# Performance work log

Hardware: AMD Instinct MI355X
Metric: run time of the kernel (lower is better)

The kernel has to match this reference:

```python
import jax, jax.numpy as jnp
import numpy as np

T, D, H, E, K = 8192, 1024, 1024, 8, 2
N = T * K  # total dispatched rows


def setup_inputs() -> dict:
    key = jax.random.key(0)
    ks = jax.random.split(key, 12)
    s = 1.0 / np.sqrt(D)
    inp = {
        # uniform, contiguous per-expert segments: 2048 rows each
        'offsets': jnp.arange(E + 1, dtype=jnp.int64 if jax.config.jax_enable_x64 else jnp.int32) * (N // E),
        'jagged': jax.random.normal(ks[0], (T, D), jnp.float32),
        'weight': jax.random.normal(ks[1], (E, D, H), jnp.float32) * s,
        'bias': jax.random.normal(ks[2], (E, H), jnp.float32) * 0.02,
        'index': jax.random.randint(ks[3], (N,), 0, T),
        'weight_p': jax.random.normal(ks[4], (E, D, H), jnp.float32) * s,
        'weight_out': jax.random.normal(ks[5], (E, H, D), jnp.float32) * (1.0 / np.sqrt(H)),
        'reverse_index': jax.random.randint(ks[6], (T, K), 0, N),
        'gates': jax.random.uniform(ks[7], (N,), jnp.float32),
        'gates_index': jax.random.randint(ks[8], (T, K), 0, N),
        'bias_p': jax.random.normal(ks[9], (E, H), jnp.float32) * 0.02,
        'bias_out': jax.random.normal(ks[10], (E, D), jnp.float32) * 0.02,
    }
    return inp


def reference(offsets, jagged, weight, bias, index, weight_p, weight_out,
              reverse_index, gates, gates_index, bias_p, bias_out):
    # dispatch: gather token features into expert-sorted order  [N, D]
    x = jagged[index]
    n = x.shape[0]
    n_experts = weight.shape[0]
    # contiguous segment id per dispatched row
    expert_id = jnp.searchsorted(offsets, jnp.arange(n), side='right') - 1
    y = jnp.zeros((n, weight_out.shape[-1]), dtype=x.dtype)
    for e in range(n_experts):  # fixed small expert count
        m = (expert_id == e)[:, None].astype(x.dtype)
        xe = x * m
        g = xe @ weight[e] + bias[e]        # gate proj  [N, H]
        u = xe @ weight_p[e] + bias_p[e]    # up proj    [N, H]
        h = jax.nn.silu(g) * u              # SwiGLU
        y = y + (h @ weight_out[e] + bias_out[e]) * m
    # combine: gather K expert outputs per token, weight by gates  [T, D]
    gathered = y[reverse_index]             # [T, K, D]
    gv = gates[gates_index]                 # [T, K]
    return jnp.einsum('tkd,tk->td', gathered, gv)
```

## Files before the change

kernel.cpp:

```cpp
#include <hip/hip_runtime.h>
#include <hip/hip_bf16.h>

#define T_TOK 8192
#define DDIM 1024
#define HDIM 1024
#define NEXP 8
#define KTOP 2
#define NROWS (T_TOK * KTOP)

typedef __attribute__((ext_vector_type(8))) short bf16x8;
typedef __attribute__((ext_vector_type(4))) float f32x4;

__device__ __forceinline__ unsigned short f2bf(float f) {
    unsigned u = __builtin_bit_cast(unsigned, f);
    u += 0x7fffu + ((u >> 16) & 1u);
    return (unsigned short)(u >> 16);
}
__device__ __forceinline__ float bf2f(unsigned short h) {
    return __builtin_bit_cast(float, (unsigned)h << 16);
}

__device__ __forceinline__ void gll16(const unsigned short* g, const unsigned short* l) {
    __builtin_amdgcn_global_load_lds(
        (const __attribute__((address_space(1))) unsigned int*)g,
        (__attribute__((address_space(3))) unsigned int*)l, 16, 0, 0);
}


__global__ __launch_bounds__(256) void cvt_bf16_k(const float* __restrict__ in,
                                                  unsigned short* __restrict__ out, int n4) {
    int i = blockIdx.x * 256 + threadIdx.x;
    if (i >= n4) return;
    float4 v = ((const float4*)in)[i];
    ushort4 o;
    o.x = f2bf(v.x); o.y = f2bf(v.y); o.z = f2bf(v.z); o.w = f2bf(v.w);
    ((ushort4*)out)[i] = o;
}

__global__ __launch_bounds__(256) void transpose_cast_k(const float* __restrict__ in,
                                                        unsigned short* __restrict__ out,
                                                        int R, int C) {
    __shared__ unsigned short tile[32][33];
    int m = blockIdx.z;
    const float* src = in + (size_t)m * R * C;
    unsigned short* dst = out + (size_t)m * R * C;
    int c0 = blockIdx.x * 32, r0 = blockIdx.y * 32;
    int tx = threadIdx.x & 31, ty = threadIdx.x >> 5;
#pragma unroll
    for (int i = 0; i < 32; i += 8)
        tile[ty + i][tx] = f2bf(src[(size_t)(r0 + ty + i) * C + c0 + tx]);
    __syncthreads();
#pragma unroll
    for (int i = 0; i < 32; i += 8)
        dst[(size_t)(c0 + ty + i) * R + r0 + tx] = tile[tx][ty + i];
}


constexpr int BM2 = 256, BN2 = 256, BK2 = 32;
constexpr int NT2 = DDIM / BK2;

template <int VARIANT>
__global__ __launch_bounds__(512) void gemm256_8p_k(
    const unsigned short* __restrict__ A, const int* __restrict__ rowidx, int lda,
    const unsigned short* __restrict__ Bt, const float* __restrict__ biasE,
    const unsigned short* __restrict__ Gin, unsigned short* __restrict__ Out,
    const int* __restrict__ offsets, int N, int K) {
    __shared__ __attribute__((aligned(16))) unsigned short lds[65536];

    const int nbn = N / BN2;
    int l = (blockIdx.x & 7) * 32 + (blockIdx.x >> 3);
    int brow = l / nbn, bcol = l % nbn;
    int row0 = brow * BM2, col0 = bcol * BN2;
    int e = 0;
    while (offsets[e + 1] <= row0) ++e;

    const unsigned short* Bte = Bt + (size_t)e * N * K;
    const float* bias = biasE + (size_t)e * N;

    int tid = threadIdx.x;
    int lane = tid & 63, wid = tid >> 6;
    int wm = wid >> 2, wn = wid & 3;
    int l15 = lane & 15, l4 = lane >> 4;

    int sc = (lane & 7) ^ (lane >> 3);
    int srow = ((lane >> 3) << 1) + (sc >> 2);
    int scol = (sc & 3) * 8;
    const unsigned short* asrc[2];
    const unsigned short* bsrc[2];
#pragma unroll
    for (int q = 0; q < 2; ++q) {
        int gr = row0 + (wid * 2 + q) * 16 + srow;
        int ar = rowidx ? rowidx[gr] : gr;
        asrc[q] = A + (size_t)ar * lda + scol;
        bsrc[q] = Bte + (size_t)(col0 + (wid * 2 + q) * 16 + srow) * K + scol;
    }
    unsigned adst[2], bdst[2];
#pragma unroll
    for (int q = 0; q < 2; ++q) {
        adst[q] = (wid * 2 + q) * 512;
        bdst[q] = 32768 + (wid * 2 + q) * 512;
    }

#define STAGE_A(t) { int _b = (t) & 3; int _k = (t) * BK2;            \
        gll16(asrc[0] + _k, lds + _b * 8192 + adst[0]);               \
        gll16(asrc[1] + _k, lds + _b * 8192 + adst[1]); }
#define STAGE_B(t) { int _b = (t) & 3; int _k = (t) * BK2;            \
        gll16(bsrc[0] + _k, lds + _b * 8192 + bdst[0]);               \
        gll16(bsrc[1] + _k, lds + _b * 8192 + bdst[1]); }

    int rdoff = (l15 >> 1) * 128 + ((((l15 & 1) << 2) | l4) ^ (l15 >> 1)) * 16;

    f32x4 acc[8][4] = {};

    STAGE_A(0) STAGE_B(0) STAGE_A(1) STAGE_B(1) STAGE_A(2) STAGE_B(2)
    asm volatile("s_waitcnt vmcnt(8)" ::: "memory");
    __builtin_amdgcn_s_barrier();

#pragma unroll 1
    for (int t = 0; t < NT2; ++t) {
        const char* Ab = (const char*)lds + (t & 3) * 16384;
        const char* Bb = (const char*)lds + 65536 + (t & 3) * 16384;
        bf16x8 af0[4], af1[4], bfr[4];

#pragma unroll
        for (int mi = 0; mi < 4; ++mi)
            af0[mi] = *(const bf16x8*)(Ab + (wm * 64 + mi * 8) * 128 + rdoff);
#pragma unroll
        for (int ni = 0; ni < 4; ++ni)
            bfr[ni] = *(const bf16x8*)(Bb + (wn * 32 + ni * 8) * 128 + rdoff);
        if (t + 3 < NT2) STAGE_A(t + 3)
        __builtin_amdgcn_s_barrier();
        asm volatile("s_waitcnt lgkmcnt(0)" ::: "memory");
        __builtin_amdgcn_sched_barrier(0);
        __builtin_amdgcn_s_setprio(1);
#pragma unroll
        for (int mi = 0; mi < 4; ++mi)
#pragma unroll
            for (int ni = 0; ni < 4; ++ni)
                acc[mi][ni] = __builtin_amdgcn_mfma_f32_16x16x32_bf16(
                    af0[mi], bfr[ni], acc[mi][ni], 0, 0, 0);
        __builtin_amdgcn_s_setprio(0);
        __builtin_amdgcn_s_barrier();

#pragma unroll
        for (int mi = 0; mi < 4; ++mi)
            af1[mi] = *(const bf16x8*)(Ab + (wm * 64 + 32 + mi * 8) * 128 + rdoff);
        if (t + 3 < NT2) STAGE_B(t + 3)
        __builtin_amdgcn_s_barrier();
        asm volatile("s_waitcnt lgkmcnt(0)" ::: "memory");
        __builtin_amdgcn_sched_barrier(0);
        __builtin_amdgcn_s_setprio(1);
#pragma unroll
        for (int mi = 0; mi < 4; ++mi)
#pragma unroll
            for (int ni = 0; ni < 4; ++ni)
                acc[4 + mi][ni] = __builtin_amdgcn_mfma_f32_16x16x32_bf16(
                    af1[mi], bfr[ni], acc[4 + mi][ni], 0, 0, 0);
        __builtin_amdgcn_s_setprio(0);

        if (t < NT2 - 1) {
            if (t <= NT2 - 4)      asm volatile("s_waitcnt vmcnt(8)" ::: "memory");
            else if (t == NT2 - 3) asm volatile("s_waitcnt vmcnt(4)" ::: "memory");
            else                   asm volatile("s_waitcnt vmcnt(0)" ::: "memory");
            __builtin_amdgcn_s_barrier();
        }
    }
#undef STAGE_A
#undef STAGE_B

    float bv[4];
#pragma unroll
    for (int ni = 0; ni < 4; ++ni)
        bv[ni] = bias[col0 + wn * 64 + ni * 16 + l15];

#pragma unroll
    for (int a = 0; a < 8; ++a) {
        int orow_b = row0 + wm * 128 + (a >> 2) * 64 + (a & 3) * 16 + l4 * 4;
#pragma unroll
        for (int ni = 0; ni < 4; ++ni) {
            int ocol = col0 + wn * 64 + ni * 16 + l15;
#pragma unroll
            for (int q = 0; q < 4; ++q) {
                size_t oidx = (size_t)(orow_b + q) * N + ocol;
                float v = acc[a][ni][q] + bv[ni];
                if (VARIANT == 1) {
                    float g = bf2f(Gin[oidx]);
                    float s = g / (1.0f + __expf(-g));
                    v = s * v;
                }
                Out[oidx] = f2bf(v);
            }
        }
    }
}


__global__ __launch_bounds__(256) void combine_k(
    const unsigned short* __restrict__ Y, const int* __restrict__ rev,
    const float* __restrict__ gates, const int* __restrict__ gidx,
    float* __restrict__ out) {
    int t = blockIdx.x;
    int r0 = rev[2 * t], r1 = rev[2 * t + 1];
    float g0 = gates[gidx[2 * t]], g1 = gates[gidx[2 * t + 1]];
    const unsigned short* y0 = Y + (size_t)r0 * DDIM;
    const unsigned short* y1 = Y + (size_t)r1 * DDIM;
    int d = threadIdx.x * 4;
    ushort4 a = *(const ushort4*)(y0 + d);
    ushort4 b = *(const ushort4*)(y1 + d);
    float4 r;
    r.x = g0 * bf2f(a.x) + g1 * bf2f(b.x);
    r.y = g0 * bf2f(a.y) + g1 * bf2f(b.y);
    r.z = g0 * bf2f(a.z) + g1 * bf2f(b.z);
    r.w = g0 * bf2f(a.w) + g1 * bf2f(b.w);
    *(float4*)(out + (size_t)t * DDIM + d) = r;
}


extern "C" void kernel_launch(void* const* d_in, const int* in_sizes, int n_in,
                              void* d_out, int out_size, void* d_ws, size_t ws_size,
                              hipStream_t stream) {
    const int* offsets = (const int*)d_in[0];
    const float* jagged = (const float*)d_in[1];
    const float* weight = (const float*)d_in[2];
    const float* bias = (const float*)d_in[3];
    const int* index = (const int*)d_in[4];
    const float* weight_p = (const float*)d_in[5];
    const float* weight_out = (const float*)d_in[6];
    const int* rev = (const int*)d_in[7];
    const float* gates = (const float*)d_in[8];
    const int* gidx = (const int*)d_in[9];
    const float* bias_p = (const float*)d_in[10];
    const float* bias_out = (const float*)d_in[11];
    float* out = (float*)d_out;

    char* w = (char*)d_ws;
    unsigned short* jag_bf = (unsigned short*)w; w += (size_t)T_TOK * DDIM * 2;
    unsigned short* W1t    = (unsigned short*)w; w += (size_t)NEXP * DDIM * HDIM * 2;
    unsigned short* Wpt    = (unsigned short*)w; w += (size_t)NEXP * DDIM * HDIM * 2;
    unsigned short* Wot    = (unsigned short*)w; w += (size_t)NEXP * HDIM * DDIM * 2;
    unsigned short* g_ws   = (unsigned short*)w; w += (size_t)NROWS * HDIM * 2;
    unsigned short* h_ws   = (unsigned short*)w; w += (size_t)NROWS * HDIM * 2;
    unsigned short* y_ws   = g_ws;

    cvt_bf16_k<<<(T_TOK * DDIM / 4 + 255) / 256, 256, 0, stream>>>(jagged, jag_bf, T_TOK * DDIM / 4);
    transpose_cast_k<<<dim3(HDIM / 32, DDIM / 32, NEXP), 256, 0, stream>>>(weight, W1t, DDIM, HDIM);
    transpose_cast_k<<<dim3(HDIM / 32, DDIM / 32, NEXP), 256, 0, stream>>>(weight_p, Wpt, DDIM, HDIM);
    transpose_cast_k<<<dim3(DDIM / 32, HDIM / 32, NEXP), 256, 0, stream>>>(weight_out, Wot, HDIM, DDIM);

    const int grid = (NROWS / BM2) * (HDIM / BN2);

    gemm256_8p_k<0><<<grid, 512, 0, stream>>>(jag_bf, index, DDIM, W1t, bias, nullptr, g_ws,
                                              offsets, HDIM, DDIM);
    gemm256_8p_k<1><<<grid, 512, 0, stream>>>(jag_bf, index, DDIM, Wpt, bias_p, g_ws, h_ws,
                                              offsets, HDIM, DDIM);
    gemm256_8p_k<0><<<grid, 512, 0, stream>>>(h_ws, nullptr, HDIM, Wot, bias_out, nullptr, y_ws,
                                              offsets, DDIM, HDIM);
    combine_k<<<T_TOK, 256, 0, stream>>>(y_ws, rev, gates, gidx, out);
}
```

Before: 183.0 us.

## Collapse two-phase ping-pong K-loop into single-barrier loop per k-tile

Replaces the 8-phase style inner loop, which split each k-tile into two half-MFMA phases with staggered A/B staging and several barriers, with a simpler loop. The new loop issues all staging loads up front, reads all 8 A fragments and 4 B fragments, runs all 32 MFMAs, and then uses one wait-and-barrier per tile. The aim is to cut barrier count and scheduling overhead. In exchange it gives up the interleaving of LDS reads, global loads and MFMAs between waves, uses more fragment registers, and may leave MFMA units idle during the LDS reads.

```diff
diff --git a/kernel.cpp b/kernel.cpp
--- a/kernel.cpp
+++ b/kernel.cpp
@@ -60,7 +60,7 @@
 constexpr int NT2 = DDIM / BK2;
 
 template <int VARIANT>
-__global__ __launch_bounds__(512) void gemm256_8p_k(
+__global__ __launch_bounds__(512) void gemm256_1b_k(
     const unsigned short* __restrict__ A, const int* __restrict__ rowidx, int lda,
     const unsigned short* __restrict__ Bt, const float* __restrict__ biasE,
     const unsigned short* __restrict__ Gin, unsigned short* __restrict__ Out,
@@ -101,10 +101,9 @@
         bdst[q] = 32768 + (wid * 2 + q) * 512;
     }
 
-#define STAGE_A(t) { int _b = (t) & 3; int _k = (t) * BK2;            \
+#define STAGE(t) { int _b = (t) & 3; int _k = (t) * BK2;              \
         gll16(asrc[0] + _k, lds + _b * 8192 + adst[0]);               \
-        gll16(asrc[1] + _k, lds + _b * 8192 + adst[1]); }
-#define STAGE_B(t) { int _b = (t) & 3; int _k = (t) * BK2;            \
+        gll16(asrc[1] + _k, lds + _b * 8192 + adst[1]);               \
         gll16(bsrc[0] + _k, lds + _b * 8192 + bdst[0]);               \
         gll16(bsrc[1] + _k, lds + _b * 8192 + bdst[1]); }
 
@@ -112,7 +111,7 @@
 
     f32x4 acc[8][4] = {};
 
-    STAGE_A(0) STAGE_B(0) STAGE_A(1) STAGE_B(1) STAGE_A(2) STAGE_B(2)
+    STAGE(0) STAGE(1) STAGE(2)
     asm volatile("s_waitcnt vmcnt(8)" ::: "memory");
     __builtin_amdgcn_s_barrier();
 
@@ -120,53 +119,32 @@
     for (int t = 0; t < NT2; ++t) {
         const char* Ab = (const char*)lds + (t & 3) * 16384;
         const char* Bb = (const char*)lds + 65536 + (t & 3) * 16384;
-        bf16x8 af0[4], af1[4], bfr[4];
-
-#pragma unroll
-        for (int mi = 0; mi < 4; ++mi)
-            af0[mi] = *(const bf16x8*)(Ab + (wm * 64 + mi * 8) * 128 + rdoff);
+        if (t + 3 < NT2) STAGE(t + 3)
+        bf16x8 af[8], bfr[4];
+#pragma unroll
+        for (int mi = 0; mi < 8; ++mi)
+            af[mi] = *(const bf16x8*)(Ab + (wm * 64 + mi * 8) * 128 + rdoff);
 #pragma unroll
         for (int ni = 0; ni < 4; ++ni)
             bfr[ni] = *(const bf16x8*)(Bb + (wn * 32 + ni * 8) * 128 + rdoff);
-        if (t + 3 < NT2) STAGE_A(t + 3)
-        __builtin_amdgcn_s_barrier();
         asm volatile("s_waitcnt lgkmcnt(0)" ::: "memory");
         __builtin_amdgcn_sched_barrier(0);
         __builtin_amdgcn_s_setprio(1);
 #pragma unroll
-        for (int mi = 0; mi < 4; ++mi)
+        for (int mi = 0; mi < 8; ++mi)
 #pragma unroll
             for (int ni = 0; ni < 4; ++ni)
                 acc[mi][ni] = __builtin_amdgcn_mfma_f32_16x16x32_bf16(
-                    af0[mi], bfr[ni], acc[mi][ni], 0, 0, 0);
+                    af[mi], bfr[ni], acc[mi][ni], 0, 0, 0);
         __builtin_amdgcn_s_setprio(0);
-        __builtin_amdgcn_s_barrier();
-
-#pragma unroll
-        for (int mi = 0; mi < 4; ++mi)
-            af1[mi] = *(const bf16x8*)(Ab + (wm * 64 + 32 + mi * 8) * 128 + rdoff);
-        if (t + 3 < NT2) STAGE_B(t + 3)
-        __builtin_amdgcn_s_barrier();
-        asm volatile("s_waitcnt lgkmcnt(0)" ::: "memory");
-        __builtin_amdgcn_sched_barrier(0);
-        __builtin_amdgcn_s_setprio(1);
-#pragma unroll
-        for (int mi = 0; mi < 4; ++mi)
-#pragma unroll
-            for (int ni = 0; ni < 4; ++ni)
-                acc[4 + mi][ni] = __builtin_amdgcn_mfma_f32_16x16x32_bf16(
-                    af1[mi], bfr[ni], acc[4 + mi][ni], 0, 0, 0);
-        __builtin_amdgcn_s_setprio(0);
-
         if (t < NT2 - 1) {
-            if (t <= NT2 - 4)      asm volatile("s_waitcnt vmcnt(8)" ::: "memory");
-            else if (t == NT2 - 3) asm volatile("s_waitcnt vmcnt(4)" ::: "memory");
+            if (t + 3 < NT2)       asm volatile("s_waitcnt vmcnt(8)" ::: "memory");
+            else if (t + 3 == NT2) asm volatile("s_waitcnt vmcnt(4)" ::: "memory");
             else                   asm volatile("s_waitcnt vmcnt(0)" ::: "memory");
             __builtin_amdgcn_s_barrier();
         }
     }
-#undef STAGE_A
-#undef STAGE_B
+#undef STAGE
 
     float bv[4];
 #pragma unroll
@@ -174,15 +152,15 @@
         bv[ni] = bias[col0 + wn * 64 + ni * 16 + l15];
 
 #pragma unroll
-    for (int a = 0; a < 8; ++a) {
-        int orow_b = row0 + wm * 128 + (a >> 2) * 64 + (a & 3) * 16 + l4 * 4;
+    for (int mi = 0; mi < 8; ++mi) {
+        int orow_b = row0 + wm * 128 + mi * 16 + l4 * 4;
 #pragma unroll
         for (int ni = 0; ni < 4; ++ni) {
             int ocol = col0 + wn * 64 + ni * 16 + l15;
 #pragma unroll
             for (int q = 0; q < 4; ++q) {
                 size_t oidx = (size_t)(orow_b + q) * N + ocol;
-                float v = acc[a][ni][q] + bv[ni];
+                float v = acc[mi][ni][q] + bv[ni];
                 if (VARIANT == 1) {
                     float g = bf2f(Gin[oidx]);
                     float s = g / (1.0f + __expf(-g));
@@ -249,11 +227,11 @@
 
     const int grid = (NROWS / BM2) * (HDIM / BN2);
 
-    gemm256_8p_k<0><<<grid, 512, 0, stream>>>(jag_bf, index, DDIM, W1t, bias, nullptr, g_ws,
+    gemm256_1b_k<0><<<grid, 512, 0, stream>>>(jag_bf, index, DDIM, W1t, bias, nullptr, g_ws,
                                               offsets, HDIM, DDIM);
-    gemm256_8p_k<1><<<grid, 512, 0, stream>>>(jag_bf, index, DDIM, Wpt, bias_p, g_ws, h_ws,
+    gemm256_1b_k<1><<<grid, 512, 0, stream>>>(jag_bf, index, DDIM, Wpt, bias_p, g_ws, h_ws,
                                               offsets, HDIM, DDIM);
-    gemm256_8p_k<0><<<grid, 512, 0, stream>>>(h_ws, nullptr, HDIM, Wot, bias_out, nullptr, y_ws,
+    gemm256_1b_k<0><<<grid, 512, 0, stream>>>(h_ws, nullptr, HDIM, Wot, bias_out, nullptr, y_ws,
                                               offsets, DDIM, HDIM);
     combine_k<<<T_TOK, 256, 0, stream>>>(y_ws, rev, gates, gidx, out);
 }
```

Measured after the change: 180.9 us. About the same (-1.1%).
